# Performance work log

Measured on AMD Instinct MI355X. Metric: run time of the kernel, lower is better.

## Reference

```python
import jax, jax.numpy as jnp
import numpy as np

N = 50000      # num nodes
E = 800000     # num edges (avg degree 16)
IN_FEA = 256
OU_FEA = 64


def setup_inputs() -> dict:
    key = jax.random.key(0)
    k_h, k_w, k_r, k_c, k_v = jax.random.split(key, 5)
    h = jax.random.normal(k_h, (N, IN_FEA), dtype=jnp.float32)
    # Linear(in_fea, ou_fea, bias=None): weight applied as h @ W, W [IN, OUT]
    W = jax.random.normal(k_w, (IN_FEA, OU_FEA), dtype=jnp.float32) / np.sqrt(IN_FEA)
    row = jax.random.randint(k_r, (E,), 0, N, dtype=jnp.int32)
    col = jax.random.randint(k_c, (E,), 0, N, dtype=jnp.int32)
    vals = jax.random.uniform(k_v, (E,), dtype=jnp.float32)
    return {"h": h, "W": W, "row": row, "col": col, "vals": vals}


def reference(h, W, row, col, vals):
    # dense projection: [N, IN] @ [IN, OUT] -> [N, OUT]
    hp = h @ W
    # torch builds sparse tensor with indices [col, row], i.e. G = A^T,
    # so torch.sparse.mm(G, hp)[i] = sum over edges with col==i of vals * hp[row]
    msg = hp[row] * vals[:, None]                      # [E, OUT] gather + scale
    out = jax.ops.segment_sum(msg, col, num_segments=N)  # scatter-add to dest
    return out
```

## Files before the change

kernel.cpp:

```cpp
#include <hip/hip_runtime.h>
#include <hip/hip_bf16.h>

#define IN_F 256
#define OU_F 64
#define BKN 128
#define BSHIFT 7
#define NBMAX 512
#define CHUNK 4096
#define STAGE_CAP 4096

typedef __attribute__((ext_vector_type(8))) short short8;
typedef __attribute__((ext_vector_type(4))) float f32x4;

__device__ inline short8 cvt8(float4 a, float4 b)
{
    union { short8 s8; __hip_bfloat162 h2[4]; } u;
    u.h2[0] = __float22bfloat162_rn(make_float2(a.x, a.y));
    u.h2[1] = __float22bfloat162_rn(make_float2(a.z, a.w));
    u.h2[2] = __float22bfloat162_rn(make_float2(b.x, b.y));
    u.h2[3] = __float22bfloat162_rn(make_float2(b.z, b.w));
    return u.s8;
}

__global__ void __launch_bounds__(512, 4)
gemm_mfma_kernel(const float* __restrict__ h, const float* __restrict__ W,
                 __hip_bfloat16* __restrict__ hp, int* __restrict__ bcnt, int N)
{
    __shared__ unsigned short Wt[64][264];
    const int t = threadIdx.x;

    if (blockIdx.x == 0)
        for (int i = t; i <= NBMAX; i += 512) bcnt[i] = 0;

#pragma unroll
    for (int i = 0; i < 16; ++i) {
        int p  = t + i * 512;
        int c  = p & 63;
        int k0 = (p >> 6) << 1;
        float x = W[(size_t)k0 * OU_F + c];
        float y = W[(size_t)(k0 + 1) * OU_F + c];
        __hip_bfloat162 bb = __float22bfloat162_rn(make_float2(x, y));
        *reinterpret_cast<unsigned*>(&Wt[c][k0]) = *reinterpret_cast<unsigned*>(&bb);
    }
    __syncthreads();

    const int l   = t & 63;
    const int wv  = t >> 6;
    const int cl  = l & 15;
    const int kg  = l >> 4;
    const int rg4 = wv & 3;
    const int cg  = wv >> 2;

    short8 bfr[2][8];
#pragma unroll
    for (int nt2 = 0; nt2 < 2; ++nt2)
#pragma unroll
        for (int ks = 0; ks < 8; ++ks)
            bfr[nt2][ks] = *reinterpret_cast<const short8*>(
                &Wt[cg * 32 + nt2 * 16 + cl][ks * 32 + kg * 8]);

    const int rbase = blockIdx.x * 64 + rg4 * 16;
    const int r     = rbase + cl;
    const int rld   = min(r, N - 1);
    const float4* hrow = reinterpret_cast<const float4*>(h) + (size_t)rld * (IN_F / 4);

    f32x4 acc0 = (f32x4){0.f, 0.f, 0.f, 0.f};
    f32x4 acc1 = (f32x4){0.f, 0.f, 0.f, 0.f};
#pragma unroll
    for (int ks = 0; ks < 8; ++ks) {
        float4 a0 = hrow[ks * 8 + kg * 2];
        float4 a1 = hrow[ks * 8 + kg * 2 + 1];
        short8 af = cvt8(a0, a1);
        acc0 = __builtin_amdgcn_mfma_f32_16x16x32_bf16(af, bfr[0][ks], acc0, 0, 0, 0);
        acc1 = __builtin_amdgcn_mfma_f32_16x16x32_bf16(af, bfr[1][ks], acc1, 0, 0, 0);
    }

#pragma unroll
    for (int rg = 0; rg < 4; ++rg) {
        int rr = rbase + kg * 4 + rg;
        if (rr < N) {
            size_t base = (size_t)rr * OU_F + cg * 32 + cl;
            hp[base]      = __float2bfloat16(acc0[rg]);
            hp[base + 16] = __float2bfloat16(acc1[rg]);
        }
    }
}

__global__ void __launch_bounds__(256)
hist_scan_kernel(const int* __restrict__ col, int* __restrict__ bcnt,
                 int* __restrict__ boffs, int* __restrict__ bcursor, int E, int NB)
{
    __shared__ int lh[NBMAX];
    __shared__ int s[256];
    __shared__ int isLast;
    const int t = threadIdx.x;

    for (int i = t; i < NB; i += 256) lh[i] = 0;
    __syncthreads();

    const int n4 = E >> 2;
    const int4* c4 = (const int4*)col;
    for (int i = blockIdx.x * 256 + t; i < n4; i += gridDim.x * 256) {
        int4 v = c4[i];
        atomicAdd(&lh[v.x >> BSHIFT], 1);
        atomicAdd(&lh[v.y >> BSHIFT], 1);
        atomicAdd(&lh[v.z >> BSHIFT], 1);
        atomicAdd(&lh[v.w >> BSHIFT], 1);
    }
    if (blockIdx.x == 0)
        for (int e = (n4 << 2) + t; e < E; e += 256)
            atomicAdd(&lh[col[e] >> BSHIFT], 1);
    __syncthreads();

    for (int i = t; i < NB; i += 256)
        if (lh[i]) atomicAdd(&bcnt[i], lh[i]);

    __threadfence();
    if (t == 0) {
        int v = atomicAdd(&bcnt[NBMAX], 1);
        isLast = (v == (int)gridDim.x - 1);
    }
    __syncthreads();
    if (!isLast) return;

    for (int i = t; i < NB; i += 256)
        lh[i] = __hip_atomic_load(&bcnt[i], __ATOMIC_RELAXED, __HIP_MEMORY_SCOPE_AGENT);
    __syncthreads();

    int idx = t * 2;
    int c0 = (idx     < NB) ? lh[idx]     : 0;
    int c1 = (idx + 1 < NB) ? lh[idx + 1] : 0;
    int s0 = c0, s1 = s0 + c1;
    s[t] = s1;
    __syncthreads();
    for (int d = 1; d < 256; d <<= 1) {
        int v = (t >= d) ? s[t - d] : 0;
        __syncthreads();
        s[t] += v;
        __syncthreads();
    }
    int excl = (t > 0) ? s[t - 1] : 0;
    if (idx     < NB) { boffs[idx]     = excl;      bcursor[idx]     = excl;      }
    if (idx + 1 < NB) { boffs[idx + 1] = excl + s0; bcursor[idx + 1] = excl + s0; }
    if (t == 255) boffs[NB] = s[255];
}

__global__ void __launch_bounds__(512)
partition_kernel(const int* __restrict__ row, const int* __restrict__ col,
                 const float* __restrict__ vals, int* __restrict__ bcursor,
                 int2* __restrict__ epk, int E, int NB)
{
    __shared__ int  hist[NBMAX];
    __shared__ int  X[NBMAX];
    __shared__ int  gshift[NBMAX];
    __shared__ int  s[256];
    __shared__ int2 stage[CHUNK];
    __shared__ int  gpos[CHUNK];

    const int t = threadIdx.x;
    const int base = blockIdx.x * CHUNK;
    const int n = min(CHUNK, E - base);

    for (int i = t; i < NBMAX; i += 512) hist[i] = 0;
    __syncthreads();

#pragma unroll
    for (int k = 0; k < CHUNK / 512; ++k) {
        int i = t + k * 512;
        if (i < n) atomicAdd(&hist[col[base + i] >> BSHIFT], 1);
    }
    __syncthreads();

    int s0 = 0, s1 = 0;
    if (t < 256) {
        int idx = t * 2;
        s0 = hist[idx];
        s1 = s0 + hist[idx + 1];
        s[t] = s1;
    }
    __syncthreads();
    for (int d = 1; d < 256; d <<= 1) {
        int v = (t >= d && t < 256) ? s[t - d] : 0;
        __syncthreads();
        if (t < 256) s[t] += v;
        __syncthreads();
    }
    if (t < 256) {
        int excl = (t > 0) ? s[t - 1] : 0;
        X[t * 2]     = excl;
        X[t * 2 + 1] = excl + s0;
    }
    __syncthreads();

    for (int i = t; i < NB; i += 512) {
        int hcnt = hist[i];
        int g = hcnt ? atomicAdd(&bcursor[i], hcnt) : 0;
        gshift[i] = g - X[i];
    }
    __syncthreads();

#pragma unroll
    for (int k = 0; k < CHUNK / 512; ++k) {
        int i = t + k * 512;
        if (i < n) {
            int e  = base + i;
            int cv = col[e];
            int b  = cv >> BSHIFT;
            int r  = atomicAdd(&X[b], 1);
            unsigned pk = (unsigned)row[e] | ((unsigned)(cv & (BKN - 1)) << 17);
            stage[r] = make_int2((int)pk, __float_as_int(vals[e]));
            gpos[r]  = gshift[b] + r;
        }
    }
    __syncthreads();

#pragma unroll
    for (int k = 0; k < CHUNK / 512; ++k) {
        int i = t + k * 512;
        if (i < n) epk[gpos[i]] = stage[i];
    }
}

__global__ void __launch_bounds__(512)
csr_kernel(const int2* __restrict__ epk, const int* __restrict__ boffs,
           int2* __restrict__ epk2, int* __restrict__ node_offs,
           int N, int NB)
{
    __shared__ int  cnt[BKN];
    __shared__ int  cur[BKN];
    __shared__ int2 stage[STAGE_CAP];
    const int t = threadIdx.x;
    const int b = blockIdx.x;
    const int s = boffs[b], e = boffs[b + 1];
    const int n = e - s;
    const int node0 = b << BSHIFT;

    if (t < BKN) cnt[t] = 0;
    __syncthreads();
    for (int i = t; i < n; i += 512)
        atomicAdd(&cnt[((unsigned)epk[s + i].x) >> 17], 1);
    __syncthreads();

    if (t < 64) {
        int v0 = cnt[2 * t], v1 = cnt[2 * t + 1];
        int p = v0 + v1, sum = p;
#pragma unroll
        for (int d = 1; d < 64; d <<= 1) {
            int u = __shfl_up(sum, d);
            if (t >= d) sum += u;
        }
        int excl = sum - p;
        cur[2 * t]     = excl;
        cur[2 * t + 1] = excl + v0;
        int nd0 = node0 + 2 * t;
        if (nd0 < N)     node_offs[nd0]     = s + excl;
        if (nd0 + 1 < N) node_offs[nd0 + 1] = s + excl + v0;
    }
    if (b == NB - 1 && t == 0) node_offs[N] = e;
    __syncthreads();

    if (n <= STAGE_CAP) {
        for (int i = t; i < n; i += 512) {
            int2 r = epk[s + i];
            int pos = atomicAdd(&cur[((unsigned)r.x) >> 17], 1);
            stage[pos] = r;
        }
        __syncthreads();
        for (int i = t; i < n; i += 512)
            epk2[s + i] = stage[i];
    } else {
        for (int i = t; i < n; i += 512) {
            int2 r = epk[s + i];
            int pos = atomicAdd(&cur[((unsigned)r.x) >> 17], 1);
            epk2[s + pos] = r;
        }
    }
}

__global__ void __launch_bounds__(256)
gather_kernel(const __hip_bfloat16* __restrict__ hp, const int* __restrict__ node_offs,
              const int2* __restrict__ epk2, float* __restrict__ out, int N)
{
    int wid  = (int)((blockIdx.x * 256u + threadIdx.x) >> 6);
    int lane = threadIdx.x & 63;
    if (wid >= N) return;
    int s = node_offs[wid], e = node_offs[wid + 1];
    float acc = 0.f;
    for (int base = s; base < e; base += 64) {
        int n = min(64, e - base);
        int2 m = make_int2(0, 0);
        if (lane < n) m = epk2[base + lane];
        int j = 0;
        for (; j + 4 <= n; j += 4) {
            unsigned r0 = (unsigned)__shfl(m.x, j)     & 0x1FFFFu;
            unsigned r1 = (unsigned)__shfl(m.x, j + 1) & 0x1FFFFu;
            unsigned r2 = (unsigned)__shfl(m.x, j + 2) & 0x1FFFFu;
            unsigned r3 = (unsigned)__shfl(m.x, j + 3) & 0x1FFFFu;
            float v0 = __int_as_float(__shfl(m.y, j));
            float v1 = __int_as_float(__shfl(m.y, j + 1));
            float v2 = __int_as_float(__shfl(m.y, j + 2));
            float v3 = __int_as_float(__shfl(m.y, j + 3));
            float x0 = __bfloat162float(hp[((size_t)r0 << 6) + lane]);
            float x1 = __bfloat162float(hp[((size_t)r1 << 6) + lane]);
            float x2 = __bfloat162float(hp[((size_t)r2 << 6) + lane]);
            float x3 = __bfloat162float(hp[((size_t)r3 << 6) + lane]);
            acc = fmaf(v0, x0, acc);
            acc = fmaf(v1, x1, acc);
            acc = fmaf(v2, x2, acc);
            acc = fmaf(v3, x3, acc);
        }
        for (; j < n; ++j) {
            unsigned r = (unsigned)__shfl(m.x, j) & 0x1FFFFu;
            float    v = __int_as_float(__shfl(m.y, j));
            acc = fmaf(v, __bfloat162float(hp[((size_t)r << 6) + lane]), acc);
        }
    }
    out[(size_t)wid * OU_F + lane] = acc;
}

__global__ void __launch_bounds__(256)
scatter_kernel(const __hip_bfloat16* __restrict__ hp, const int* __restrict__ row,
               const int* __restrict__ col, const float* __restrict__ vals,
               float* __restrict__ out, int E)
{
    unsigned int gid = blockIdx.x * 256u + threadIdx.x;
    int e = (int)(gid >> 6);
    if (e >= E) return;
    int f = (int)(gid & 63u);
    int r = row[e], c = col[e];
    float m = vals[e] * __bfloat162float(hp[(size_t)r * OU_F + f]);
    __hip_atomic_fetch_add(&out[(size_t)c * OU_F + f], m,
                           __ATOMIC_RELAXED, __HIP_MEMORY_SCOPE_AGENT);
}

extern "C" void kernel_launch(void* const* d_in, const int* in_sizes, int n_in,
                              void* d_out, int out_size, void* d_ws, size_t ws_size,
                              hipStream_t stream)
{
    const float* h    = (const float*)d_in[0];
    const float* W    = (const float*)d_in[1];
    const int*   row  = (const int*)d_in[2];
    const int*   col  = (const int*)d_in[3];
    const float* vals = (const float*)d_in[4];
    float*       out  = (float*)d_out;

    const int N = in_sizes[0] / IN_F;
    const int E = in_sizes[2];
    const int NB = (N + BKN - 1) / BKN;

    char*  ws  = (char*)d_ws;
    size_t off = 0;
    auto alloc = [&](size_t bytes) -> char* {
        char* p = ws + off;
        off = (off + bytes + 255) & ~(size_t)255;
        return p;
    };
    __hip_bfloat16* hp = (__hip_bfloat16*)alloc((size_t)N * OU_F * 2);
    int*   bcnt      = (int*)  alloc((size_t)(NBMAX + 1) * 4);
    int*   boffs     = (int*)  alloc((size_t)(NBMAX + 1) * 4);
    int*   bcursor   = (int*)  alloc((size_t)NBMAX * 4);
    int*   node_offs = (int*)  alloc((size_t)(N + 1) * 4);
    int2*  epk       = (int2*) alloc((size_t)E * 8);
    int2*  epk2      = (int2*) alloc((size_t)E * 8);
    const bool fits = (off <= ws_size) && (NB <= NBMAX) && (N < 131072);

    const int ntiles = (N + 63) / 64;
    gemm_mfma_kernel<<<ntiles, 512, 0, stream>>>(h, W, hp, bcnt, N);

    if (fits) {
        hist_scan_kernel<<<256, 256, 0, stream>>>(col, bcnt, boffs, bcursor, E, NB);
        partition_kernel<<<(E + CHUNK - 1) / CHUNK, 512, 0, stream>>>(
            row, col, vals, bcursor, epk, E, NB);
        csr_kernel<<<NB, 512, 0, stream>>>(epk, boffs, epk2, node_offs, N, NB);
        gather_kernel<<<(N + 3) / 4, 256, 0, stream>>>(hp, node_offs, epk2, out, N);
    } else {
        hipMemsetAsync(d_out, 0, (size_t)out_size * sizeof(float), stream);
        unsigned long long total = (unsigned long long)E * 64ull;
        unsigned int sgrid = (unsigned int)((total + 255ull) / 256ull);
        scatter_kernel<<<sgrid, 256, 0, stream>>>(hp, row, col, vals, out, E);
    }
}
```

Measured before the change: 90.00 us.

## Fuse histogram/scan into GEMM launch and shrink partition chunks with segment copies

Merges the column histogram and bucket scan into the GEMM kernel as extra blocks, so the two run concurrently in one launch. Each GEMM block now processes two 64-row tiles. Bucket counter zeroing moves to a memset. The partition kernel halves its chunk size, drops the gpos array, and writes bucket segments contiguously per wave for better coalescing and occupancy. This adds a memset launch, and the union shared memory keeps GEMM blocks at the same footprint.

```diff
diff --git a/kernel.cpp b/kernel.cpp
--- a/kernel.cpp
+++ b/kernel.cpp
@@ -6,8 +6,9 @@
 #define BKN 128
 #define BSHIFT 7
 #define NBMAX 512
-#define CHUNK 4096
+#define PCHUNK 2048
 #define STAGE_CAP 4096
+#define NHIST 64
 
 typedef __attribute__((ext_vector_type(8))) short short8;
 typedef __attribute__((ext_vector_type(4))) float f32x4;
@@ -23,15 +24,75 @@
 }
 
 __global__ void __launch_bounds__(512, 4)
-gemm_mfma_kernel(const float* __restrict__ h, const float* __restrict__ W,
-                 __hip_bfloat16* __restrict__ hp, int* __restrict__ bcnt, int N)
-{
-    __shared__ unsigned short Wt[64][264];
-    const int t = threadIdx.x;
-
-    if (blockIdx.x == 0)
-        for (int i = t; i <= NBMAX; i += 512) bcnt[i] = 0;
-
+fused_gemm_hist(const float* __restrict__ h, const float* __restrict__ W,
+                __hip_bfloat16* __restrict__ hp, const int* __restrict__ col,
+                int* __restrict__ bcnt, int* __restrict__ boffs,
+                int* __restrict__ bcursor, int N, int E, int NB)
+{
+    union Sh {
+        unsigned short Wt[64][264];
+        struct { int lh[NBMAX]; int s[256]; } hh;
+    };
+    __shared__ Sh sh;
+    __shared__ int isLast;
+    const int t   = threadIdx.x;
+    const int bid = blockIdx.x;
+
+    if (bid < NHIST) {
+        for (int i = t; i < NBMAX; i += 512) sh.hh.lh[i] = 0;
+        __syncthreads();
+        const int n4 = E >> 2;
+        const int4* c4 = (const int4*)col;
+        for (int i = bid * 512 + t; i < n4; i += NHIST * 512) {
+            int4 v = c4[i];
+            atomicAdd(&sh.hh.lh[v.x >> BSHIFT], 1);
+            atomicAdd(&sh.hh.lh[v.y >> BSHIFT], 1);
+            atomicAdd(&sh.hh.lh[v.z >> BSHIFT], 1);
+            atomicAdd(&sh.hh.lh[v.w >> BSHIFT], 1);
+        }
+        if (bid == 0)
+            for (int e = (n4 << 2) + t; e < E; e += 512)
+                atomicAdd(&sh.hh.lh[col[e] >> BSHIFT], 1);
+        __syncthreads();
+        for (int i = t; i < NB; i += 512)
+            if (sh.hh.lh[i]) atomicAdd(&bcnt[i], sh.hh.lh[i]);
+        __threadfence();
+        __syncthreads();
+        if (t == 0) {
+            int v = atomicAdd(&bcnt[NBMAX], 1);
+            isLast = (v == NHIST - 1);
+        }
+        __syncthreads();
+        if (!isLast) return;
+
+        for (int i = t; i < NB; i += 512)
+            sh.hh.lh[i] = __hip_atomic_load(&bcnt[i], __ATOMIC_RELAXED,
+                                            __HIP_MEMORY_SCOPE_AGENT);
+        __syncthreads();
+        int s0 = 0, s1 = 0;
+        if (t < 256) {
+            s0 = sh.hh.lh[2 * t];
+            s1 = s0 + sh.hh.lh[2 * t + 1];
+            sh.hh.s[t] = s1;
+        }
+        __syncthreads();
+        for (int d = 1; d < 256; d <<= 1) {
+            int v = (t < 256 && t >= d) ? sh.hh.s[t - d] : 0;
+            __syncthreads();
+            if (t < 256) sh.hh.s[t] += v;
+            __syncthreads();
+        }
+        if (t < 256) {
+            int excl = t ? sh.hh.s[t - 1] : 0;
+            int i0 = 2 * t, i1 = 2 * t + 1;
+            if (i0 < NB) { boffs[i0] = excl;      bcursor[i0] = excl;      }
+            if (i1 < NB) { boffs[i1] = excl + s0; bcursor[i1] = excl + s0; }
+            if (t == 255) boffs[NB] = sh.hh.s[255];
+        }
+        return;
+    }
+
+    const int tb = bid - NHIST;
 #pragma unroll
     for (int i = 0; i < 16; ++i) {
         int p  = t + i * 512;
@@ -40,7 +101,7 @@
         float x = W[(size_t)k0 * OU_F + c];
         float y = W[(size_t)(k0 + 1) * OU_F + c];
         __hip_bfloat162 bb = __float22bfloat162_rn(make_float2(x, y));
-        *reinterpret_cast<unsigned*>(&Wt[c][k0]) = *reinterpret_cast<unsigned*>(&bb);
+        *reinterpret_cast<unsigned*>(&sh.Wt[c][k0]) = *reinterpret_cast<unsigned*>(&bb);
     }
     __syncthreads();
 
@@ -57,95 +118,38 @@
 #pragma unroll
         for (int ks = 0; ks < 8; ++ks)
             bfr[nt2][ks] = *reinterpret_cast<const short8*>(
-                &Wt[cg * 32 + nt2 * 16 + cl][ks * 32 + kg * 8]);
-
-    const int rbase = blockIdx.x * 64 + rg4 * 16;
-    const int r     = rbase + cl;
-    const int rld   = min(r, N - 1);
-    const float4* hrow = reinterpret_cast<const float4*>(h) + (size_t)rld * (IN_F / 4);
-
-    f32x4 acc0 = (f32x4){0.f, 0.f, 0.f, 0.f};
-    f32x4 acc1 = (f32x4){0.f, 0.f, 0.f, 0.f};
-#pragma unroll
-    for (int ks = 0; ks < 8; ++ks) {
-        float4 a0 = hrow[ks * 8 + kg * 2];
-        float4 a1 = hrow[ks * 8 + kg * 2 + 1];
-        short8 af = cvt8(a0, a1);
-        acc0 = __builtin_amdgcn_mfma_f32_16x16x32_bf16(af, bfr[0][ks], acc0, 0, 0, 0);
-        acc1 = __builtin_amdgcn_mfma_f32_16x16x32_bf16(af, bfr[1][ks], acc1, 0, 0, 0);
-    }
-
-#pragma unroll
-    for (int rg = 0; rg < 4; ++rg) {
-        int rr = rbase + kg * 4 + rg;
-        if (rr < N) {
-            size_t base = (size_t)rr * OU_F + cg * 32 + cl;
-            hp[base]      = __float2bfloat16(acc0[rg]);
-            hp[base + 16] = __float2bfloat16(acc1[rg]);
-        }
-    }
-}
-
-__global__ void __launch_bounds__(256)
-hist_scan_kernel(const int* __restrict__ col, int* __restrict__ bcnt,
-                 int* __restrict__ boffs, int* __restrict__ bcursor, int E, int NB)
-{
-    __shared__ int lh[NBMAX];
-    __shared__ int s[256];
-    __shared__ int isLast;
-    const int t = threadIdx.x;
-
-    for (int i = t; i < NB; i += 256) lh[i] = 0;
-    __syncthreads();
-
-    const int n4 = E >> 2;
-    const int4* c4 = (const int4*)col;
-    for (int i = blockIdx.x * 256 + t; i < n4; i += gridDim.x * 256) {
-        int4 v = c4[i];
-        atomicAdd(&lh[v.x >> BSHIFT], 1);
-        atomicAdd(&lh[v.y >> BSHIFT], 1);
-        atomicAdd(&lh[v.z >> BSHIFT], 1);
-        atomicAdd(&lh[v.w >> BSHIFT], 1);
-    }
-    if (blockIdx.x == 0)
-        for (int e = (n4 << 2) + t; e < E; e += 256)
-            atomicAdd(&lh[col[e] >> BSHIFT], 1);
-    __syncthreads();
-
-    for (int i = t; i < NB; i += 256)
-        if (lh[i]) atomicAdd(&bcnt[i], lh[i]);
-
-    __threadfence();
-    if (t == 0) {
-        int v = atomicAdd(&bcnt[NBMAX], 1);
-        isLast = (v == (int)gridDim.x - 1);
-    }
-    __syncthreads();
-    if (!isLast) return;
-
-    for (int i = t; i < NB; i += 256)
-        lh[i] = __hip_atomic_load(&bcnt[i], __ATOMIC_RELAXED, __HIP_MEMORY_SCOPE_AGENT);
-    __syncthreads();
-
-    int idx = t * 2;
-    int c0 = (idx     < NB) ? lh[idx]     : 0;
-    int c1 = (idx + 1 < NB) ? lh[idx + 1] : 0;
-    int s0 = c0, s1 = s0 + c1;
-    s[t] = s1;
-    __syncthreads();
-    for (int d = 1; d < 256; d <<= 1) {
-        int v = (t >= d) ? s[t - d] : 0;
-        __syncthreads();
-        s[t] += v;
-        __syncthreads();
-    }
-    int excl = (t > 0) ? s[t - 1] : 0;
-    if (idx     < NB) { boffs[idx]     = excl;      bcursor[idx]     = excl;      }
-    if (idx + 1 < NB) { boffs[idx + 1] = excl + s0; bcursor[idx + 1] = excl + s0; }
-    if (t == 255) boffs[NB] = s[255];
-}
-
-__global__ void __launch_bounds__(512)
+                &sh.Wt[cg * 32 + nt2 * 16 + cl][ks * 32 + kg * 8]);
+
+#pragma unroll
+    for (int tt = 0; tt < 2; ++tt) {
+        const int rbase = tb * 128 + tt * 64 + rg4 * 16;
+        const int r     = rbase + cl;
+        const int rld   = min(r, N - 1);
+        const float4* hrow = reinterpret_cast<const float4*>(h) + (size_t)rld * (IN_F / 4);
+
+        f32x4 acc0 = (f32x4){0.f, 0.f, 0.f, 0.f};
+        f32x4 acc1 = (f32x4){0.f, 0.f, 0.f, 0.f};
+#pragma unroll
+        for (int ks = 0; ks < 8; ++ks) {
+            float4 a0 = hrow[ks * 8 + kg * 2];
+            float4 a1 = hrow[ks * 8 + kg * 2 + 1];
+            short8 af = cvt8(a0, a1);
+            acc0 = __builtin_amdgcn_mfma_f32_16x16x32_bf16(af, bfr[0][ks], acc0, 0, 0, 0);
+            acc1 = __builtin_amdgcn_mfma_f32_16x16x32_bf16(af, bfr[1][ks], acc1, 0, 0, 0);
+        }
+#pragma unroll
+        for (int rg = 0; rg < 4; ++rg) {
+            int rr = rbase + kg * 4 + rg;
+            if (rr < N) {
+                size_t base = (size_t)rr * OU_F + cg * 32 + cl;
+                hp[base]      = __float2bfloat16(acc0[rg]);
+                hp[base + 16] = __float2bfloat16(acc1[rg]);
+            }
+        }
+    }
+}
+
+__global__ void __launch_bounds__(512, 4)
 partition_kernel(const int* __restrict__ row, const int* __restrict__ col,
                  const float* __restrict__ vals, int* __restrict__ bcursor,
                  int2* __restrict__ epk, int E, int NB)
@@ -154,53 +158,51 @@
     __shared__ int  X[NBMAX];
     __shared__ int  gshift[NBMAX];
     __shared__ int  s[256];
-    __shared__ int2 stage[CHUNK];
-    __shared__ int  gpos[CHUNK];
+    __shared__ int2 stage[PCHUNK];
 
     const int t = threadIdx.x;
-    const int base = blockIdx.x * CHUNK;
-    const int n = min(CHUNK, E - base);
+    const int base = blockIdx.x * PCHUNK;
+    const int n = min(PCHUNK, E - base);
 
     for (int i = t; i < NBMAX; i += 512) hist[i] = 0;
     __syncthreads();
 
 #pragma unroll
-    for (int k = 0; k < CHUNK / 512; ++k) {
+    for (int k = 0; k < PCHUNK / 512; ++k) {
         int i = t + k * 512;
         if (i < n) atomicAdd(&hist[col[base + i] >> BSHIFT], 1);
     }
     __syncthreads();
 
-    int s0 = 0, s1 = 0;
+    int h0 = 0, h1 = 0;
     if (t < 256) {
-        int idx = t * 2;
-        s0 = hist[idx];
-        s1 = s0 + hist[idx + 1];
-        s[t] = s1;
+        h0 = hist[2 * t];
+        h1 = h0 + hist[2 * t + 1];
+        s[t] = h1;
     }
     __syncthreads();
     for (int d = 1; d < 256; d <<= 1) {
-        int v = (t >= d && t < 256) ? s[t - d] : 0;
+        int v = (t < 256 && t >= d) ? s[t - d] : 0;
         __syncthreads();
         if (t < 256) s[t] += v;
         __syncthreads();
     }
     if (t < 256) {
-        int excl = (t > 0) ? s[t - 1] : 0;
-        X[t * 2]     = excl;
-        X[t * 2 + 1] = excl + s0;
+        int excl = t ? s[t - 1] : 0;
+        X[2 * t]     = excl;
+        X[2 * t + 1] = excl + h0;
     }
     __syncthreads();
 
     for (int i = t; i < NB; i += 512) {
-        int hcnt = hist[i];
-        int g = hcnt ? atomicAdd(&bcursor[i], hcnt) : 0;
+        int hc = hist[i];
+        int g = hc ? atomicAdd(&bcursor[i], hc) : 0;
         gshift[i] = g - X[i];
     }
     __syncthreads();
 
 #pragma unroll
-    for (int k = 0; k < CHUNK / 512; ++k) {
+    for (int k = 0; k < PCHUNK / 512; ++k) {
         int i = t + k * 512;
         if (i < n) {
             int e  = base + i;
@@ -209,15 +211,18 @@
             int r  = atomicAdd(&X[b], 1);
             unsigned pk = (unsigned)row[e] | ((unsigned)(cv & (BKN - 1)) << 17);
             stage[r] = make_int2((int)pk, __float_as_int(vals[e]));
-            gpos[r]  = gshift[b] + r;
-        }
-    }
-    __syncthreads();
-
-#pragma unroll
-    for (int k = 0; k < CHUNK / 512; ++k) {
-        int i = t + k * 512;
-        if (i < n) epk[gpos[i]] = stage[i];
+        }
+    }
+    __syncthreads();
+
+    const int l = t & 63, wv = t >> 6;
+    for (int b = wv; b < NB; b += 8) {
+        int cnt = hist[b];
+        if (!cnt) continue;
+        int src0 = X[b] - cnt;
+        int dst0 = gshift[b] + src0;
+        for (int j = l; j < cnt; j += 64)
+            epk[dst0 + j] = stage[src0 + j];
     }
 }
 
@@ -364,16 +369,20 @@
     int2*  epk2      = (int2*) alloc((size_t)E * 8);
     const bool fits = (off <= ws_size) && (NB <= NBMAX) && (N < 131072);
 
-    const int ntiles = (N + 63) / 64;
-    gemm_mfma_kernel<<<ntiles, 512, 0, stream>>>(h, W, hp, bcnt, N);
+    const int ntiles2 = (N + 127) / 128;
 
     if (fits) {
-        hist_scan_kernel<<<256, 256, 0, stream>>>(col, bcnt, boffs, bcursor, E, NB);
-        partition_kernel<<<(E + CHUNK - 1) / CHUNK, 512, 0, stream>>>(
+        hipMemsetAsync(bcnt, 0, (size_t)(NBMAX + 1) * 4, stream);
+        fused_gemm_hist<<<NHIST + ntiles2, 512, 0, stream>>>(
+            h, W, hp, col, bcnt, boffs, bcursor, N, E, NB);
+        partition_kernel<<<(E + PCHUNK - 1) / PCHUNK, 512, 0, stream>>>(
             row, col, vals, bcursor, epk, E, NB);
         csr_kernel<<<NB, 512, 0, stream>>>(epk, boffs, epk2, node_offs, N, NB);
         gather_kernel<<<(N + 3) / 4, 256, 0, stream>>>(hp, node_offs, epk2, out, N);
     } else {
+        hipMemsetAsync(bcnt, 0, (size_t)(NBMAX + 1) * 4, stream);
+        fused_gemm_hist<<<NHIST + ntiles2, 512, 0, stream>>>(
+            h, W, hp, col, bcnt, boffs, bcursor, N, E, NB);
         hipMemsetAsync(d_out, 0, (size_t)out_size * sizeof(float), stream);
         unsigned long long total = (unsigned long long)E * 64ull;
         unsigned int sgrid = (unsigned int)((total + 255ull) / 256ull);
```

Result: slower. 105.3 us (+17.0%).
